# Kernel optimization log

Measured on AMD Instinct MI355X. Metric: run time of the kernel, lower is better.

Reference implementation:

```python
import jax, jax.numpy as jnp
import numpy as np
import math

MAX_REL_POS = 32  # max_relative_position

def _sincos_table(d_model, max_len):
    pos = np.arange(max_len)[:, None].astype(np.float32)
    div = np.exp(np.arange(0, d_model, 2).astype(np.float32) * (-math.log(10000.0) / d_model))
    pe = np.zeros((max_len, d_model), dtype=np.float32)
    pe[:, 0::2] = np.sin(pos * div)
    pe[:, 1::2] = np.cos(pos * div)
    return jnp.asarray(pe)

def setup_inputs() -> dict:
    rng = jax.random.key(0)
    k1, k2, k3 = jax.random.split(rng, 3)
    B, H, S, D = 4, 16, 1024, 64
    pe = _sincos_table(D, 2 * MAX_REL_POS + 1)  # fixed (non-trainable) buffer
    return {
        "query": jax.random.normal(k1, (B, H, S, D), jnp.float32),
        "key": jax.random.normal(k2, (B, H, S, D), jnp.float32),
        "value": jax.random.normal(k3, (B, H, S, D), jnp.float32),
        "pe_k": pe,
        "pe_v": pe,
    }

def reference(query, key, value, pe_k, pe_v):
    B, H, S, D = query.shape
    # relative distance indices: clip(k - q, -P, P) + P  -> [S, S]
    dist = jnp.clip(jnp.arange(S)[None, :] - jnp.arange(S)[:, None],
                    -MAX_REL_POS, MAX_REL_POS) + MAX_REL_POS
    R_k = pe_k[dist]  # [S, S, D]
    R_v = pe_v[dist]  # [S, S, D]
    scores = jnp.einsum('bhqd,bhkd->bhqk', query, key)
    scores = scores + jnp.einsum('bhqd,qkd->bhqk', query, R_k)
    scores = scores / math.sqrt(D)
    # one_direction=True -> causal mask
    causal = jnp.tril(jnp.ones((S, S), dtype=bool))
    scores = jnp.where(causal[None, None], scores, jnp.float32(-1e9))
    p_attn = jax.nn.softmax(scores, axis=-1)
    output = jnp.einsum('bhqk,bhkd->bhqd', p_attn, value)
    output = output + jnp.einsum('bhqv,qvd->bhqd', p_attn, R_v)
    return output, p_attn
```

## Files before the change

### kernel.cpp

```cpp
#include <hip/hip_runtime.h>

typedef __attribute__((ext_vector_type(8))) short bfrag;
typedef __attribute__((ext_vector_type(4))) float ffrag;

namespace {
constexpr int Sc = 1024, Dc = 64;
constexpr int P2 = 72;
constexpr int PQ = 64;
constexpr int PW = 33;
constexpr float SCALE = 0.125f;
}

__device__ __forceinline__ unsigned short f2bf(float f) {
    unsigned u = __builtin_bit_cast(unsigned, f);
    u += 0x7fffu + ((u >> 16) & 1u);
    return (unsigned short)(u >> 16);
}
__device__ __forceinline__ bfrag pack8(float4 a, float4 b) {
    bfrag r;
    r[0] = (short)f2bf(a.x); r[1] = (short)f2bf(a.y);
    r[2] = (short)f2bf(a.z); r[3] = (short)f2bf(a.w);
    r[4] = (short)f2bf(b.x); r[5] = (short)f2bf(b.y);
    r[6] = (short)f2bf(b.z); r[7] = (short)f2bf(b.w);
    return r;
}
#define MFMA(a, b, c) __builtin_amdgcn_mfma_f32_16x16x32_bf16((a), (b), (c), 0, 0, 0)

__global__ __launch_bounds__(256, 3)
void relattn(const float* __restrict__ Qg, const float* __restrict__ Kg,
             const float* __restrict__ Vg, const float* __restrict__ pek,
             const float* __restrict__ pev, float* __restrict__ outg,
             float* __restrict__ pbuf)
{
    __shared__ __align__(16) char smem[54016];
    unsigned short* Ks0 = (unsigned short*)smem;
    unsigned short* Ks1 = (unsigned short*)(smem + 9216);
    unsigned short* Vt  = (unsigned short*)(smem + 18432);
    unsigned short* Pt  = (unsigned short*)(smem + 27648);
    float* Ts = (float*)(smem + 36864);
    unsigned short* Qs = (unsigned short*)(smem + 45312);
    float* Ws = (float*)(smem + 45312);
    float* W0 = (float*)(smem + 53760);
    float* Ot = (float*)smem;

    const int tid  = threadIdx.x;
    const int bh   = blockIdx.y;
    const int wv   = tid >> 6;
    const int lane = tid & 63;
    const int n    = lane & 15;
    const int quad = lane >> 4;

    const float* Qbh = Qg + (size_t)bh * Sc * Dc;
    const float* Kbh = Kg + (size_t)bh * Sc * Dc;
    const float* Vbh = Vg + (size_t)bh * Sc * Dc;
    float* pbh = pbuf + (size_t)bh * Sc * Sc;
    float* obh = outg + (size_t)bh * Sc * Dc;

    const int sr  = tid >> 2;
    const int sc4 = (tid & 3) * 16;
    const int kp  = tid & 31;
    const int vd0 = (tid >> 5) * 8;

    const int rr = tid >> 4;
    const int c4 = tid & 15;

    for (int half = 0; half < 2; ++half) {
        const int qt = half ? (15 - (int)blockIdx.x) : (int)blockIdx.x;
        const int qrow = wv * 16 + quad * 4;

        __syncthreads();

        float4 k0a, k0b, k0c, k0d;
        {
            const float* ksrc = Kbh + (size_t)sr * Dc + sc4;
            k0a = *(const float4*)(ksrc);
            k0b = *(const float4*)(ksrc + 4);
            k0c = *(const float4*)(ksrc + 8);
            k0d = *(const float4*)(ksrc + 12);
        }
        {
            const float* src = Qbh + (size_t)(qt * 64 + sr) * Dc + sc4;
            float4 a = *(const float4*)(src);
            float4 b = *(const float4*)(src + 4);
            float4 c = *(const float4*)(src + 8);
            float4 d = *(const float4*)(src + 12);
            *(bfrag*)&Qs[sr * PQ + sc4]     = pack8(a, b);
            *(bfrag*)&Qs[sr * PQ + sc4 + 8] = pack8(c, d);
        }
        for (int i = tid; i < 135; i += 256) {
            bfrag z = {};
            *(bfrag*)&Ks0[33 * P2 + i * 8] = z;
        }
        if (tid < 132) {
            int r = tid >> 2, c0 = (tid & 3) * 16;
            const float* src = pek + (size_t)r * Dc + c0;
            float4 a = *(const float4*)(src);
            float4 b = *(const float4*)(src + 4);
            float4 c = *(const float4*)(src + 8);
            float4 d = *(const float4*)(src + 12);
            *(bfrag*)&Ks0[r * P2 + c0]     = pack8(a, b);
            *(bfrag*)&Ks0[r * P2 + c0 + 8] = pack8(c, d);
        }
        __syncthreads();

        bfrag qa0 = *(bfrag*)&Qs[(wv * 16 + n) * PQ + quad * 8];
        bfrag qa1 = *(bfrag*)&Qs[(wv * 16 + n) * PQ + 32 + quad * 8];

        #pragma unroll
        for (int sub = 0; sub < 3; ++sub) {
            bfrag b0 = *(bfrag*)&Ks0[(sub * 16 + n) * P2 + quad * 8];
            bfrag b1 = *(bfrag*)&Ks0[(sub * 16 + n) * P2 + 32 + quad * 8];
            ffrag c = {};
            c = MFMA(qa0, b0, c);
            c = MFMA(qa1, b1, c);
            int j = sub * 16 + n;
            if (j <= 32) {
                #pragma unroll
                for (int reg = 0; reg < 4; ++reg)
                    Ts[(qrow + reg) * PW + j] = c[reg];
            }
        }
        *(bfrag*)&Ks1[sr * P2 + sc4]     = pack8(k0a, k0b);
        *(bfrag*)&Ks1[sr * P2 + sc4 + 8] = pack8(k0c, k0d);
        float4 pka, pkb, pkc, pkd;
        if (qt >= 1) {
            const float* ksrc = Kbh + (size_t)(64 + sr) * Dc + sc4;
            pka = *(const float4*)(ksrc);
            pkb = *(const float4*)(ksrc + 4);
            pkc = *(const float4*)(ksrc + 8);
            pkd = *(const float4*)(ksrc + 12);
        }
        __syncthreads();

        float ts0[4];
        #pragma unroll
        for (int reg = 0; reg < 4; ++reg) ts0[reg] = Ts[(qrow + reg) * PW];

        for (int idx = tid; idx < 64 * PW; idx += 256) Ws[idx] = 0.f;

        {
            const int zb = (qt + 1) * 64;
            if (zb < Sc) {
                const int z4 = (Sc - zb) >> 2;
                const float4 z = make_float4(0.f, 0.f, 0.f, 0.f);
                for (int r = 0; r < 64; ++r) {
                    float4* rp = (float4*)(pbh + (size_t)(qt * 64 + r) * Sc + zb);
                    for (int cz = tid; cz < z4; cz += 256) rp[cz] = z;
                }
            }
        }

        float lsum[4] = {0.f, 0.f, 0.f, 0.f};
        for (int kt = 0; kt <= qt; ++kt) {
            const bool bnd = (kt >= qt - 1);
            unsigned short* Kc = (kt & 1) ? Ks0 : Ks1;
            unsigned short* Kn = (kt & 1) ? Ks1 : Ks0;
            #pragma unroll
            for (int sub = 0; sub < 4; ++sub) {
                bfrag b0 = *(bfrag*)&Kc[(sub * 16 + n) * P2 + quad * 8];
                bfrag b1 = *(bfrag*)&Kc[(sub * 16 + n) * P2 + 32 + quad * 8];
                ffrag c = {};
                c = MFMA(qa0, b0, c);
                c = MFMA(qa1, b1, c);
                const int k = kt * 64 + sub * 16 + n;
                if (!bnd) {
                    #pragma unroll
                    for (int reg = 0; reg < 4; ++reg)
                        lsum[reg] += __expf((c[reg] + ts0[reg]) * SCALE);
                } else {
                    #pragma unroll
                    for (int reg = 0; reg < 4; ++reg) {
                        int jrel = k - (qt * 64 + qrow + reg) + 32;
                        if (jrel <= 32) {
                            int jcl = jrel < 0 ? 0 : jrel;
                            lsum[reg] += __expf((c[reg] + Ts[(qrow + reg) * PW + jcl]) * SCALE);
                        }
                    }
                }
            }
            if (kt < qt) {
                *(bfrag*)&Kn[sr * P2 + sc4]     = pack8(pka, pkb);
                *(bfrag*)&Kn[sr * P2 + sc4 + 8] = pack8(pkc, pkd);
            }
            if (kt + 2 <= qt) {
                const float* ksrc = Kbh + (size_t)((kt + 2) * 64 + sr) * Dc + sc4;
                pka = *(const float4*)(ksrc);
                pkb = *(const float4*)(ksrc + 4);
                pkc = *(const float4*)(ksrc + 8);
                pkd = *(const float4*)(ksrc + 12);
            }
            __syncthreads();
        }
        float rinv[4];
        #pragma unroll
        for (int reg = 0; reg < 4; ++reg) {
            float l = lsum[reg];
            l += __shfl_xor(l, 1);
            l += __shfl_xor(l, 2);
            l += __shfl_xor(l, 4);
            l += __shfl_xor(l, 8);
            rinv[reg] = 1.f / l;
        }

        {
            const float* ksrc = Kbh + (size_t)sr * Dc + sc4;
            float4 a = *(const float4*)(ksrc);
            float4 b = *(const float4*)(ksrc + 4);
            float4 c = *(const float4*)(ksrc + 8);
            float4 d = *(const float4*)(ksrc + 12);
            *(bfrag*)&Ks0[sr * P2 + sc4]     = pack8(a, b);
            *(bfrag*)&Ks0[sr * P2 + sc4 + 8] = pack8(c, d);
        }
        if (qt >= 1) {
            const float* ksrc = Kbh + (size_t)(64 + sr) * Dc + sc4;
            pka = *(const float4*)(ksrc);
            pkb = *(const float4*)(ksrc + 4);
            pkc = *(const float4*)(ksrc + 8);
            pkd = *(const float4*)(ksrc + 12);
        }
        float4 pva, pvb, pvc, pvd;
        {
            const float* vsrc = Vbh + (size_t)(2 * kp) * Dc + vd0;
            pva = *(const float4*)(vsrc);
            pvb = *(const float4*)(vsrc + 4);
            pvc = *(const float4*)(vsrc + Dc);
            pvd = *(const float4*)(vsrc + Dc + 4);
        }
        __syncthreads();

        ffrag oacc[4];
        #pragma unroll
        for (int i = 0; i < 4; ++i) { ffrag z = {}; oacc[i] = z; }

        for (int kt = 0; kt <= qt; ++kt) {
            const bool bnd = (kt >= qt - 1);
            unsigned short* Kc = (kt & 1) ? Ks1 : Ks0;
            unsigned short* Kn = (kt & 1) ? Ks0 : Ks1;

            #pragma unroll
            for (int sub = 0; sub < 4; ++sub) {
                bfrag b0 = *(bfrag*)&Kc[(sub * 16 + n) * P2 + quad * 8];
                bfrag b1 = *(bfrag*)&Kc[(sub * 16 + n) * P2 + 32 + quad * 8];
                ffrag c = {};
                c = MFMA(qa0, b0, c);
                c = MFMA(qa1, b1, c);
                const int k = kt * 64 + sub * 16 + n;
                if (!bnd) {
                    #pragma unroll
                    for (int reg = 0; reg < 4; ++reg) {
                        float p = __expf((c[reg] + ts0[reg]) * SCALE) * rinv[reg];
                        Pt[(qrow + reg) * P2 + sub * 16 + n] = (unsigned short)f2bf(p);
                    }
                } else {
                    #pragma unroll
                    for (int reg = 0; reg < 4; ++reg) {
                        int jrel = k - (qt * 64 + qrow + reg) + 32;
                        float p = 0.f;
                        if (jrel <= 32) {
                            int jcl = jrel < 0 ? 0 : jrel;
                            p = __expf((c[reg] + Ts[(qrow + reg) * PW + jcl]) * SCALE) * rinv[reg];
                        }
                        Pt[(qrow + reg) * P2 + sub * 16 + n] = (unsigned short)f2bf(p);
                        if ((unsigned)(jrel - 1) < 32u) Ws[(qrow + reg) * PW + jrel - 1] = p;
                    }
                }
            }
            if (kt < qt) {
                *(bfrag*)&Kn[sr * P2 + sc4]     = pack8(pka, pkb);
                *(bfrag*)&Kn[sr * P2 + sc4 + 8] = pack8(pkc, pkd);
            }
            {
                float r0[8] = {pva.x, pva.y, pva.z, pva.w, pvb.x, pvb.y, pvb.z, pvb.w};
                float r1[8] = {pvc.x, pvc.y, pvc.z, pvc.w, pvd.x, pvd.y, pvd.z, pvd.w};
                #pragma unroll
                for (int i = 0; i < 8; ++i) {
                    unsigned pk = (unsigned)f2bf(r0[i]) | ((unsigned)f2bf(r1[i]) << 16);
                    *(unsigned*)&Vt[(vd0 + i) * P2 + 2 * kp] = pk;
                }
            }
            if (kt + 2 <= qt) {
                const float* ksrc = Kbh + (size_t)((kt + 2) * 64 + sr) * Dc + sc4;
                pka = *(const float4*)(ksrc);
                pkb = *(const float4*)(ksrc + 4);
                pkc = *(const float4*)(ksrc + 8);
                pkd = *(const float4*)(ksrc + 12);
            }
            if (kt < qt) {
                const float* vsrc = Vbh + (size_t)((kt + 1) * 64 + 2 * kp) * Dc + vd0;
                pva = *(const float4*)(vsrc);
                pvb = *(const float4*)(vsrc + 4);
                pvc = *(const float4*)(vsrc + Dc);
                pvd = *(const float4*)(vsrc + Dc + 4);
            }
            __syncthreads();
            bfrag pb0 = *(bfrag*)&Pt[(wv * 16 + n) * P2 + quad * 8];
            bfrag pb1 = *(bfrag*)&Pt[(wv * 16 + n) * P2 + 32 + quad * 8];
            #pragma unroll
            for (int ds = 0; ds < 4; ++ds) {
                bfrag va0 = *(bfrag*)&Vt[(ds * 16 + n) * P2 + quad * 8];
                bfrag va1 = *(bfrag*)&Vt[(ds * 16 + n) * P2 + 32 + quad * 8];
                oacc[ds] = MFMA(va0, pb0, oacc[ds]);
                oacc[ds] = MFMA(va1, pb1, oacc[ds]);
            }
            {
                float* base = pbh + ((size_t)(qt * 64 + rr) * Sc + kt * 64 + c4 * 4);
                #pragma unroll
                for (int step = 0; step < 4; ++step) {
                    const int r = step * 16 + rr;
                    const unsigned short* ps = &Pt[r * P2 + c4 * 4];
                    unsigned two0 = *(const unsigned*)(ps);
                    unsigned two1 = *(const unsigned*)(ps + 2);
                    float4 v;
                    v.x = __builtin_bit_cast(float, (two0 & 0xffffu) << 16);
                    v.y = __builtin_bit_cast(float, two0 & 0xffff0000u);
                    v.z = __builtin_bit_cast(float, (two1 & 0xffffu) << 16);
                    v.w = __builtin_bit_cast(float, two1 & 0xffff0000u);
                    *(float4*)(base + (size_t)(step * 16) * Sc) = v;
                }
            }
            __syncthreads();
        }

        if (tid < 64) {
            float s = 0.f;
            #pragma unroll
            for (int j = 0; j < 32; ++j) s += Ws[tid * PW + j];
            W0[tid] = 1.f - s;
        }
        {
            int q = tid >> 2, j0 = (tid & 3) * 8;
            #pragma unroll
            for (int i = 0; i < 8; i += 2) {
                unsigned pk = (unsigned)f2bf(Ws[q * PW + j0 + i]) |
                              ((unsigned)f2bf(Ws[q * PW + j0 + i + 1]) << 16);
                *(unsigned*)&Pt[q * P2 + j0 + i] = pk;
            }
        }
        {
            int jj = tid >> 3, d0 = (tid & 7) * 8;
            const float* src = pev + (size_t)(jj + 1) * Dc + d0;
            float4 a = *(const float4*)(src);
            float4 b = *(const float4*)(src + 4);
            float vr[8] = {a.x, a.y, a.z, a.w, b.x, b.y, b.z, b.w};
            #pragma unroll
            for (int i = 0; i < 8; ++i)
                Vt[(d0 + i) * P2 + jj] = (unsigned short)f2bf(vr[i]);
        }
        __syncthreads();
        {
            bfrag pb = *(bfrag*)&Pt[(wv * 16 + n) * P2 + quad * 8];
            #pragma unroll
            for (int ds = 0; ds < 4; ++ds) {
                bfrag va = *(bfrag*)&Vt[(ds * 16 + n) * P2 + quad * 8];
                oacc[ds] = MFMA(va, pb, oacc[ds]);
            }
        }
        float w0q = W0[wv * 16 + n];
        #pragma unroll
        for (int ds = 0; ds < 4; ++ds) {
            float4 ov;
            ov.x = oacc[ds][0] + w0q * pev[ds * 16 + quad * 4 + 0];
            ov.y = oacc[ds][1] + w0q * pev[ds * 16 + quad * 4 + 1];
            ov.z = oacc[ds][2] + w0q * pev[ds * 16 + quad * 4 + 2];
            ov.w = oacc[ds][3] + w0q * pev[ds * 16 + quad * 4 + 3];
            *(float4*)&Ot[(wv * 16 + n) * 68 + ds * 16 + quad * 4] = ov;
        }
        __syncthreads();
        {
            int r = tid >> 2, c0 = (tid & 3) * 16;
            float* dst = obh + (size_t)(qt * 64 + r) * Dc + c0;
            *(float4*)(dst)      = *(float4*)&Ot[r * 68 + c0];
            *(float4*)(dst + 4)  = *(float4*)&Ot[r * 68 + c0 + 4];
            *(float4*)(dst + 8)  = *(float4*)&Ot[r * 68 + c0 + 8];
            *(float4*)(dst + 12) = *(float4*)&Ot[r * 68 + c0 + 12];
        }
    }
}

extern "C" void kernel_launch(void* const* d_in, const int* in_sizes, int n_in,
                              void* d_out, int out_size, void* d_ws, size_t ws_size,
                              hipStream_t stream)
{
    const float* Q   = (const float*)d_in[0];
    const float* K   = (const float*)d_in[1];
    const float* V   = (const float*)d_in[2];
    const float* pek = (const float*)d_in[3];
    const float* pev = (const float*)d_in[4];
    float* out  = (float*)d_out;
    float* pbuf = out + (size_t)64 * Sc * Dc;

    dim3 grid(8, 64);
    relattn<<<grid, 256, 0, stream>>>(Q, K, V, pek, pev, out, pbuf);
}
```

Before: 384.2 us.

## Double-buffer V and P tiles to drop one barrier per key tile

Double-buffers the V-transpose and P tiles in shared memory so the PV MFMA and the probability write-back for tile kt-1 run in the same phase as the QK^T and softmax for tile kt. This removes one __syncthreads per iteration and lets the two phases overlap. A tail step handles the final tile. Shared memory grows to about 72 KB and launch bounds drop from 3 to 2 blocks per CU, so occupancy goes down.

```diff
diff --git a/kernel.cpp b/kernel.cpp
--- a/kernel.cpp
+++ b/kernel.cpp
@@ -26,21 +26,23 @@
 }
 #define MFMA(a, b, c) __builtin_amdgcn_mfma_f32_16x16x32_bf16((a), (b), (c), 0, 0, 0)
 
-__global__ __launch_bounds__(256, 3)
+__global__ __launch_bounds__(256, 2)
 void relattn(const float* __restrict__ Qg, const float* __restrict__ Kg,
              const float* __restrict__ Vg, const float* __restrict__ pek,
              const float* __restrict__ pev, float* __restrict__ outg,
              float* __restrict__ pbuf)
 {
-    __shared__ __align__(16) char smem[54016];
+    __shared__ __align__(16) char smem[72448];
     unsigned short* Ks0 = (unsigned short*)smem;
     unsigned short* Ks1 = (unsigned short*)(smem + 9216);
-    unsigned short* Vt  = (unsigned short*)(smem + 18432);
-    unsigned short* Pt  = (unsigned short*)(smem + 27648);
-    float* Ts = (float*)(smem + 36864);
-    unsigned short* Qs = (unsigned short*)(smem + 45312);
-    float* Ws = (float*)(smem + 45312);
-    float* W0 = (float*)(smem + 53760);
+    unsigned short* Vt0 = (unsigned short*)(smem + 18432);
+    unsigned short* Vt1 = (unsigned short*)(smem + 27648);
+    unsigned short* Pt0 = (unsigned short*)(smem + 36864);
+    unsigned short* Pt1 = (unsigned short*)(smem + 46080);
+    float* Ts = (float*)(smem + 55296);
+    unsigned short* Qs = (unsigned short*)(smem + 63744);
+    float* Ws = (float*)(smem + 63744);
+    float* W0 = (float*)(smem + 72192);
     float* Ot = (float*)smem;
 
     const int tid  = threadIdx.x;
@@ -234,8 +236,12 @@
 
         for (int kt = 0; kt <= qt; ++kt) {
             const bool bnd = (kt >= qt - 1);
-            unsigned short* Kc = (kt & 1) ? Ks1 : Ks0;
-            unsigned short* Kn = (kt & 1) ? Ks0 : Ks1;
+            unsigned short* Kc  = (kt & 1) ? Ks1 : Ks0;
+            unsigned short* Kn  = (kt & 1) ? Ks0 : Ks1;
+            unsigned short* Vc  = (kt & 1) ? Vt1 : Vt0;
+            unsigned short* Vp  = (kt & 1) ? Vt0 : Vt1;
+            unsigned short* Ptc = (kt & 1) ? Pt1 : Pt0;
+            unsigned short* Ptp = (kt & 1) ? Pt0 : Pt1;
 
             #pragma unroll
             for (int sub = 0; sub < 4; ++sub) {
@@ -249,7 +255,7 @@
                     #pragma unroll
                     for (int reg = 0; reg < 4; ++reg) {
                         float p = __expf((c[reg] + ts0[reg]) * SCALE) * rinv[reg];
-                        Pt[(qrow + reg) * P2 + sub * 16 + n] = (unsigned short)f2bf(p);
+                        Ptc[(qrow + reg) * P2 + sub * 16 + n] = (unsigned short)f2bf(p);
                     }
                 } else {
                     #pragma unroll
@@ -260,7 +266,7 @@
                             int jcl = jrel < 0 ? 0 : jrel;
                             p = __expf((c[reg] + Ts[(qrow + reg) * PW + jcl]) * SCALE) * rinv[reg];
                         }
-                        Pt[(qrow + reg) * P2 + sub * 16 + n] = (unsigned short)f2bf(p);
+                        Ptc[(qrow + reg) * P2 + sub * 16 + n] = (unsigned short)f2bf(p);
                         if ((unsigned)(jrel - 1) < 32u) Ws[(qrow + reg) * PW + jrel - 1] = p;
                     }
                 }
@@ -275,7 +281,7 @@
                 #pragma unroll
                 for (int i = 0; i < 8; ++i) {
                     unsigned pk = (unsigned)f2bf(r0[i]) | ((unsigned)f2bf(r1[i]) << 16);
-                    *(unsigned*)&Vt[(vd0 + i) * P2 + 2 * kp] = pk;
+                    *(unsigned*)&Vc[(vd0 + i) * P2 + 2 * kp] = pk;
                 }
             }
             if (kt + 2 <= qt) {
@@ -285,29 +291,28 @@
                 pkc = *(const float4*)(ksrc + 8);
                 pkd = *(const float4*)(ksrc + 12);
             }
-            if (kt < qt) {
+            if (kt + 1 <= qt) {
                 const float* vsrc = Vbh + (size_t)((kt + 1) * 64 + 2 * kp) * Dc + vd0;
                 pva = *(const float4*)(vsrc);
                 pvb = *(const float4*)(vsrc + 4);
                 pvc = *(const float4*)(vsrc + Dc);
                 pvd = *(const float4*)(vsrc + Dc + 4);
             }
-            __syncthreads();
-            bfrag pb0 = *(bfrag*)&Pt[(wv * 16 + n) * P2 + quad * 8];
-            bfrag pb1 = *(bfrag*)&Pt[(wv * 16 + n) * P2 + 32 + quad * 8];
-            #pragma unroll
-            for (int ds = 0; ds < 4; ++ds) {
-                bfrag va0 = *(bfrag*)&Vt[(ds * 16 + n) * P2 + quad * 8];
-                bfrag va1 = *(bfrag*)&Vt[(ds * 16 + n) * P2 + 32 + quad * 8];
-                oacc[ds] = MFMA(va0, pb0, oacc[ds]);
-                oacc[ds] = MFMA(va1, pb1, oacc[ds]);
-            }
-            {
-                float* base = pbh + ((size_t)(qt * 64 + rr) * Sc + kt * 64 + c4 * 4);
+            if (kt >= 1) {
+                bfrag pb0 = *(bfrag*)&Ptp[(wv * 16 + n) * P2 + quad * 8];
+                bfrag pb1 = *(bfrag*)&Ptp[(wv * 16 + n) * P2 + 32 + quad * 8];
+                #pragma unroll
+                for (int ds = 0; ds < 4; ++ds) {
+                    bfrag va0 = *(bfrag*)&Vp[(ds * 16 + n) * P2 + quad * 8];
+                    bfrag va1 = *(bfrag*)&Vp[(ds * 16 + n) * P2 + 32 + quad * 8];
+                    oacc[ds] = MFMA(va0, pb0, oacc[ds]);
+                    oacc[ds] = MFMA(va1, pb1, oacc[ds]);
+                }
+                float* base = pbh + ((size_t)(qt * 64 + rr) * Sc + (kt - 1) * 64 + c4 * 4);
                 #pragma unroll
                 for (int step = 0; step < 4; ++step) {
                     const int r = step * 16 + rr;
-                    const unsigned short* ps = &Pt[r * P2 + c4 * 4];
+                    const unsigned short* ps = &Ptp[r * P2 + c4 * 4];
                     unsigned two0 = *(const unsigned*)(ps);
                     unsigned two1 = *(const unsigned*)(ps + 2);
                     float4 v;
@@ -320,6 +325,34 @@
             }
             __syncthreads();
         }
+        {
+            unsigned short* Ptp = (qt & 1) ? Pt1 : Pt0;
+            unsigned short* Vp  = (qt & 1) ? Vt1 : Vt0;
+            bfrag pb0 = *(bfrag*)&Ptp[(wv * 16 + n) * P2 + quad * 8];
+            bfrag pb1 = *(bfrag*)&Ptp[(wv * 16 + n) * P2 + 32 + quad * 8];
+            #pragma unroll
+            for (int ds = 0; ds < 4; ++ds) {
+                bfrag va0 = *(bfrag*)&Vp[(ds * 16 + n) * P2 + quad * 8];
+                bfrag va1 = *(bfrag*)&Vp[(ds * 16 + n) * P2 + 32 + quad * 8];
+                oacc[ds] = MFMA(va0, pb0, oacc[ds]);
+                oacc[ds] = MFMA(va1, pb1, oacc[ds]);
+            }
+            float* base = pbh + ((size_t)(qt * 64 + rr) * Sc + qt * 64 + c4 * 4);
+            #pragma unroll
+            for (int step = 0; step < 4; ++step) {
+                const int r = step * 16 + rr;
+                const unsigned short* ps = &Ptp[r * P2 + c4 * 4];
+                unsigned two0 = *(const unsigned*)(ps);
+                unsigned two1 = *(const unsigned*)(ps + 2);
+                float4 v;
+                v.x = __builtin_bit_cast(float, (two0 & 0xffffu) << 16);
+                v.y = __builtin_bit_cast(float, two0 & 0xffff0000u);
+                v.z = __builtin_bit_cast(float, (two1 & 0xffffu) << 16);
+                v.w = __builtin_bit_cast(float, two1 & 0xffff0000u);
+                *(float4*)(base + (size_t)(step * 16) * Sc) = v;
+            }
+        }
+        __syncthreads();
 
         if (tid < 64) {
             float s = 0.f;
@@ -333,7 +366,7 @@
             for (int i = 0; i < 8; i += 2) {
                 unsigned pk = (unsigned)f2bf(Ws[q * PW + j0 + i]) |
                               ((unsigned)f2bf(Ws[q * PW + j0 + i + 1]) << 16);
-                *(unsigned*)&Pt[q * P2 + j0 + i] = pk;
+                *(unsigned*)&Pt0[q * P2 + j0 + i] = pk;
             }
         }
         {
@@ -344,14 +377,14 @@
             float vr[8] = {a.x, a.y, a.z, a.w, b.x, b.y, b.z, b.w};
             #pragma unroll
             for (int i = 0; i < 8; ++i)
-                Vt[(d0 + i) * P2 + jj] = (unsigned short)f2bf(vr[i]);
-        }
-        __syncthreads();
-        {
-            bfrag pb = *(bfrag*)&Pt[(wv * 16 + n) * P2 + quad * 8];
+                Vt0[(d0 + i) * P2 + jj] = (unsigned short)f2bf(vr[i]);
+        }
+        __syncthreads();
+        {
+            bfrag pb = *(bfrag*)&Pt0[(wv * 16 + n) * P2 + quad * 8];
             #pragma unroll
             for (int ds = 0; ds < 4; ++ds) {
-                bfrag va = *(bfrag*)&Vt[(ds * 16 + n) * P2 + quad * 8];
+                bfrag va = *(bfrag*)&Vt0[(ds * 16 + n) * P2 + quad * 8];
                 oacc[ds] = MFMA(va, pb, oacc[ds]);
             }
         }
```

After: 373.8 us. 1.03x faster.
